# Optimization experiments

Measured on AMD Instinct MI355X. Metric: run time of the kernel, lower is better.

Reference implementation:

```python
import jax, jax.numpy as jnp
import numpy as np

N_ELEC = 8192   # electrons (nodes)
N_NUC = 512     # nuclei
EMB = 256       # embedding_dim
KER = 256       # kernel_dim
DF = 64         # dist_feat_dim
MID = 128       # round(sqrt(DF*KER)), log-interpolated hidden width of w-MLP
E = 131072      # edges per edge type


def _ssp(x):
    # shifted softplus, deepqmc default activation: log(0.5*exp(x) + 0.5)
    return jax.nn.softplus(x) - jnp.log(2.0)


def setup_inputs() -> dict:
    key = jax.random.key(0)
    ks = jax.random.split(key, 24)
    def nrm(k, shape, scale):
        return jax.random.normal(k, shape, dtype=jnp.float32) * scale
    inp = {}
    inp['electrons'] = nrm(ks[0], (N_ELEC, EMB), 1.0)
    inp['nuclei'] = nrm(ks[1], (N_NUC, KER), 1.0)
    for i, lbl in enumerate(['same', 'anti', 'n']):
        inp[f'dist_{lbl}'] = jax.random.uniform(ks[2 + i], (E, DF), dtype=jnp.float32)
        inp[f'w1_{lbl}'] = nrm(ks[5 + i], (DF, MID), DF ** -0.5)
        inp[f'b1_{lbl}'] = jnp.zeros((MID,), jnp.float32)
        inp[f'w2_{lbl}'] = nrm(ks[8 + i], (MID, KER), MID ** -0.5)
        inp[f'g_{lbl}'] = nrm(ks[11 + i], (KER, EMB), KER ** -0.5)
    inp['h_w'] = nrm(ks[14], (EMB, KER), EMB ** -0.5)
    inp['senders_same'] = jax.random.randint(ks[15], (E,), 0, N_ELEC)
    inp['senders_anti'] = jax.random.randint(ks[16], (E,), 0, N_ELEC)
    inp['senders_n'] = jax.random.randint(ks[17], (E,), 0, N_NUC)
    inp['receivers_same'] = jax.random.randint(ks[18], (E,), 0, N_ELEC)
    inp['receivers_anti'] = jax.random.randint(ks[19], (E,), 0, N_ELEC)
    inp['receivers_n'] = jax.random.randint(ks[20], (E,), 0, N_ELEC)
    return inp


def reference(electrons, nuclei, dist_same, dist_anti, dist_n,
              w1_same, b1_same, w2_same, w1_anti, b1_anti, w2_anti,
              w1_n, b1_n, w2_n, g_same, g_anti, g_n, h_w,
              senders_same, senders_anti, senders_n,
              receivers_same, receivers_anti, receivers_n):
    def w_mlp(d, w1, b1, w2):
        # MLP with ('log', 2) hidden layers: linear+bias -> SSP -> last linear (no bias)
        return _ssp(d @ w1 + b1) @ w2

    # per-edge filters from distance features: [E, KER]
    we_same = w_mlp(dist_same, w1_same, b1_same, w2_same)
    we_anti = w_mlp(dist_anti, w1_anti, b1_anti, w2_anti)
    we_n = w_mlp(dist_n, w1_n, b1_n, w2_n)

    # shared h (single bias-free linear) on gathered sender electrons: [E, KER]
    hx_same = electrons[senders_same] @ h_w
    hx_anti = electrons[senders_anti] @ h_w

    weh_same = we_same * hx_same
    weh_anti = we_anti * hx_anti
    weh_n = we_n * nuclei[senders_n]

    # scatter-sum messages to receiver electrons: [N_ELEC, KER]
    z_same = jax.ops.segment_sum(weh_same, receivers_same, num_segments=N_ELEC)
    z_anti = jax.ops.segment_sum(weh_anti, receivers_anti, num_segments=N_ELEC)
    z_n = jax.ops.segment_sum(weh_n, receivers_n, num_segments=N_ELEC)

    # per-label g (single bias-free linear) + residual update, order matches original
    return electrons + (z_n @ g_n + z_same @ g_same + z_anti @ g_anti)
```

## Files before the change

### kernel.cpp

```cpp
#include <hip/hip_runtime.h>
#include <stdint.h>


#define N_ELEC 8192
#define N_NUC  512
#define EMB    256
#define KER    256
#define DF     64
#define MID    128
#define NEDGE  131072
#define RPS    8256
#define CSTR   272

using u16 = unsigned short;
typedef short short8 __attribute__((ext_vector_type(8)));
typedef float f32x4 __attribute__((ext_vector_type(4)));

__device__ __forceinline__ float bf2f(u16 h) {
  return __uint_as_float(((unsigned)h) << 16);
}
__device__ __forceinline__ u16 f2bf(float f) {
  unsigned u = __float_as_uint(f);
  return (u16)((u + 0x7FFFu + ((u >> 16) & 1u)) >> 16);
}
__device__ __forceinline__ unsigned pkbf(float a, float b) {
  return ((unsigned)f2bf(b) << 16) | (unsigned)f2bf(a);
}
__device__ __forceinline__ float ssp_fast(float x) {
  const float e = __expf(-fabsf(x));
  return fmaxf(x, 0.f) + __logf(fmaf(0.5f, e, 0.5f));
}

__device__ __forceinline__ void stage_t64(const char* g0, long stride,
                                          char* lds, int tid) {
  const int l = tid & 63, w = tid >> 6;
  const int r = w * 16 + (l >> 2);
  const int cb = (l & 3) * 16;
  __builtin_amdgcn_global_load_lds(
      (const __attribute__((address_space(1))) unsigned*)(g0 +
                                                          (long)r * stride +
                                                          cb),
      (__attribute__((address_space(3))) unsigned*)(lds + w * 1024), 16, 0, 0);
}
__device__ __forceinline__ void stage_f64(const float* g0, int stride_e,
                                          int kt, char* lds, int tid) {
#pragma unroll
  for (int k = 0; k < 4; ++k) {
    const int idx2 = k * 256 + tid;
    const int row = idx2 >> 4, cp = idx2 & 15;
    const float2 v = *(const float2*)(g0 + (long)row * stride_e + kt + cp * 2);
    *(unsigned*)(lds + row * 64 + cp * 4) = pkbf(v.x, v.y);
  }
}
template <bool A_F32>
__device__ __forceinline__ void gemm64(const char* A0, long as_bytes,
                                       const float* Af, int as_elems,
                                       const char* B0, long bs, int K,
                                       char* As, char* Bs, f32x4 acc[2][2],
                                       int tid) {
  const int l = tid & 63, lane15 = l & 15, quad = l >> 4, wv = tid >> 6;
  const int mw = (wv >> 1) * 32, nw = (wv & 1) * 32;
  for (int kt = 0; kt < K; kt += 32) {
    if (A_F32)
      stage_f64(Af, as_elems, kt, As, tid);
    else
      stage_t64(A0 + (long)kt * 2, as_bytes, As, tid);
    stage_t64(B0 + (long)kt * 2, bs, Bs, tid);
    __syncthreads();
    short8 af[2], bf[2];
#pragma unroll
    for (int i = 0; i < 2; ++i) {
      af[i] = *(const short8*)(As + (mw + i * 16 + lane15) * 64 + quad * 16);
      bf[i] = *(const short8*)(Bs + (nw + i * 16 + lane15) * 64 + quad * 16);
    }
#pragma unroll
    for (int mi = 0; mi < 2; ++mi)
#pragma unroll
      for (int ni = 0; ni < 2; ++ni)
        acc[mi][ni] = __builtin_amdgcn_mfma_f32_16x16x32_bf16(
            af[mi], bf[ni], acc[mi][ni], 0, 0, 0);
    __syncthreads();
  }
}

__global__ __launch_bounds__(256) void k_zero2(float4* z, int* cnt) {
  const int b = blockIdx.x;
  if (b < 6144)
    z[b * 256 + threadIdx.x] = (float4){0.f, 0.f, 0.f, 0.f};
  else
    cnt[(b - 6144) * 256 + threadIdx.x] = 0;
}

__global__ __launch_bounds__(256) void k_hist(const int* r0, const int* r1,
                                              const int* r2, int* cnt) {
  const int t = blockIdx.z;
  const int* rcv = t == 0 ? r0 : (t == 1 ? r1 : r2);
  const int e = blockIdx.x * 256 + threadIdx.x;
  atomicAdd(&cnt[t * N_ELEC + rcv[e]], 1);
}

__global__ __launch_bounds__(256) void k_scan(const int* cnt, int* rowptr,
                                              int* cursor) {
  const int t = blockIdx.x, tid = threadIdx.x;
  __shared__ int part[256];
  const int* c = cnt + t * N_ELEC;
  int s = 0;
#pragma unroll
  for (int i = 0; i < 32; ++i) s += c[tid * 32 + i];
  part[tid] = s;
  __syncthreads();
  for (int off = 1; off < 256; off <<= 1) {
    int v = (tid >= off) ? part[tid - off] : 0;
    __syncthreads();
    part[tid] += v;
    __syncthreads();
  }
  int run = (tid == 0) ? 0 : part[tid - 1];
  int* rp = rowptr + t * RPS;
  int* cu = cursor + t * N_ELEC;
  for (int i = 0; i < 32; ++i) {
    rp[tid * 32 + i] = run;
    cu[tid * 32 + i] = run;
    run += c[tid * 32 + i];
  }
  if (tid == 255) rp[N_ELEC] = run;
}

__global__ __launch_bounds__(256) void k_place(const int* r0, const int* r1,
                                               const int* r2, const int* s0,
                                               const int* s1, const int* s2,
                                               int* cursor, int* perm,
                                               int* snd_s, int* rcv_s) {
  const int t = blockIdx.z;
  const int* rcv = t == 0 ? r0 : (t == 1 ? r1 : r2);
  const int* snd = t == 0 ? s0 : (t == 1 ? s1 : s2);
  const int e = blockIdx.x * 256 + threadIdx.x;
  const int rr = rcv[e];
  const int pos = atomicAdd(&cursor[t * N_ELEC + rr], 1);
  perm[t * NEDGE + pos] = e;
  snd_s[t * NEDGE + pos] = snd[e];
  rcv_s[t * NEDGE + pos] = rr;
}

__global__ __launch_bounds__(256) void k_prep(
    const float* h_w, const float* w1s, const float* w1a, const float* w1n,
    const float* w2s, const float* w2a, const float* w2n, const float* gs,
    const float* ga, const float* gn, u16* hwT, u16* w1T, u16* w2T, u16* gT) {
  int i = blockIdx.x * 256 + threadIdx.x;
  if (i < 65536) {
    int n = i >> 8, k = i & 255;
    hwT[i] = f2bf(h_w[k * 256 + n]);
    return;
  }
  int j = i - 65536;
  if (j < 24576) {
    int t = j >> 13, jj = j & 8191, n = jj >> 6, k = jj & 63;
    const float* w1 = t == 0 ? w1s : (t == 1 ? w1a : w1n);
    w1T[j] = f2bf(w1[k * 128 + n]);
    return;
  }
  j -= 24576;
  if (j < 98304) {
    int t = j >> 15, jj = j & 32767, n = jj >> 7, k = jj & 127;
    const float* w2 = t == 0 ? w2s : (t == 1 ? w2a : w2n);
    w2T[j] = f2bf(w2[k * 256 + n]);
    return;
  }
  j -= 98304;
  if (j < 196608) {
    int n = j / 768, q = j % 768, t = q >> 8, k = q & 255;
    const float* g = t == 0 ? gs : (t == 1 ? ga : gn);
    gT[j] = f2bf(g[k * 256 + n]);
  }
}

__global__ __launch_bounds__(256) void k_he(const float* elec, const u16* hwT,
                                            u16* he) {
  __shared__ char As[4096], Bs[4096];
  f32x4 acc[2][2];
#pragma unroll
  for (int i = 0; i < 2; ++i)
#pragma unroll
    for (int j = 0; j < 2; ++j) acc[i][j] = (f32x4){0.f, 0.f, 0.f, 0.f};
  const int m0 = blockIdx.x * 64, n0 = blockIdx.y * 64;
  gemm64<true>(nullptr, 0, elec + (long)m0 * 256, 256,
               (const char*)hwT + (long)n0 * 512, 512, 256, As, Bs, acc,
               threadIdx.x);
  const int l = threadIdx.x & 63, lane15 = l & 15, quad = l >> 4,
            wv = threadIdx.x >> 6;
  const int mw = (wv >> 1) * 32, nw = (wv & 1) * 32;
#pragma unroll
  for (int mi = 0; mi < 2; ++mi)
#pragma unroll
    for (int r = 0; r < 4; ++r) {
      const int row = m0 + mw + mi * 16 + quad * 4 + r;
#pragma unroll
      for (int ni = 0; ni < 2; ++ni) {
        const int col = n0 + nw + ni * 16 + lane15;
        he[row * 256 + col] = f2bf(acc[mi][ni][r]);
      }
    }
}

__global__ __launch_bounds__(256, 3) void k_edge(
    const float* d0, const float* d1, const float* d2, const float* b0,
    const float* b1p, const float* b2, const u16* w1T, const u16* w2T,
    const u16* he, const float* nucf, const int* perm, const int* snd_s,
    const int* rcv_s, float* z) {
  __shared__ char buf[128 * CSTR];
  __shared__ int snd_l[128], rcv_l[128];

  const int t = blockIdx.z;
  const int m0 = blockIdx.x * 128;
  const int tid = threadIdx.x;
  const float* dist = t == 0 ? d0 : (t == 1 ? d1 : d2);
  const float* bias = t == 0 ? b0 : (t == 1 ? b1p : b2);
  const u16* w1t = w1T + t * 8192;
  const u16* w2t = w2T + t * 32768;
  const bool is_nuc = (t == 2);

  if (tid < 128)
    snd_l[tid] = snd_s[t * NEDGE + m0 + tid];
  else
    rcv_l[tid - 128] = rcv_s[t * NEDGE + m0 + tid - 128];

  int rows[4];
  const int* pm = perm + t * NEDGE + m0;
#pragma unroll
  for (int s = 0; s < 4; ++s) rows[s] = pm[(s * 256 + tid) >> 3];
#pragma unroll
  for (int j = 0; j < 2; ++j)
#pragma unroll
    for (int s = 0; s < 4; ++s) {
      const int idx = s * 256 + tid, row = idx >> 3, ch = idx & 7;
      const float4 v =
          *(const float4*)(dist + (long)rows[s] * 64 + j * 32 + ch * 4);
      uint2 p;
      p.x = pkbf(v.x, v.y);
      p.y = pkbf(v.z, v.w);
      *(uint2*)(buf + j * 8192 + row * 64 + ch * 8) = p;
    }
  __syncthreads();

  const int l = tid & 63, lane15 = l & 15, quad = l >> 4, wv = tid >> 6;
  const int mw = (wv >> 1) * 64, nw = (wv & 1) * 64;

  f32x4 acc[4][4];
#pragma unroll
  for (int i = 0; i < 4; ++i)
#pragma unroll
    for (int j = 0; j < 4; ++j) acc[i][j] = (f32x4){0.f, 0.f, 0.f, 0.f};
#pragma unroll
  for (int j = 0; j < 2; ++j) {
    short8 af[4], bf[4];
#pragma unroll
    for (int i = 0; i < 4; ++i) {
      af[i] = *(const short8*)(buf + j * 8192 + (mw + i * 16 + lane15) * 64 +
                               quad * 16);
      bf[i] = *(const short8*)(w1t + (nw + i * 16 + lane15) * 64 + j * 32 +
                               quad * 8);
    }
#pragma unroll
    for (int mi = 0; mi < 4; ++mi)
#pragma unroll
      for (int ni = 0; ni < 4; ++ni)
        acc[mi][ni] = __builtin_amdgcn_mfma_f32_16x16x32_bf16(
            af[mi], bf[ni], acc[mi][ni], 0, 0, 0);
  }
  __syncthreads();

#pragma unroll
  for (int mi = 0; mi < 4; ++mi)
#pragma unroll
    for (int r = 0; r < 4; ++r) {
      const int row = mw + mi * 16 + quad * 4 + r;
#pragma unroll
      for (int ni = 0; ni < 4; ++ni) {
        const int col = nw + ni * 16 + lane15;
        const float x = acc[mi][ni][r] + bias[col];
        *(u16*)(buf + row * CSTR + col * 2) = f2bf(ssp_fast(x));
      }
    }
  __syncthreads();

  short8 afr[4][4];
#pragma unroll
  for (int j = 0; j < 4; ++j)
#pragma unroll
    for (int i = 0; i < 4; ++i)
      afr[j][i] = *(const short8*)(buf + (mw + i * 16 + lane15) * CSTR +
                                   j * 64 + quad * 16);
  __syncthreads();

  u16* HeC = (u16*)buf;
  for (int n0 = 0; n0 < 256; n0 += 128) {
#pragma unroll
    for (int i = 0; i < 4; ++i)
#pragma unroll
      for (int j = 0; j < 4; ++j) acc[i][j] = (f32x4){0.f, 0.f, 0.f, 0.f};
#pragma unroll
    for (int j = 0; j < 4; ++j) {
      short8 bf[4];
#pragma unroll
      for (int i = 0; i < 4; ++i)
        bf[i] = *(const short8*)(w2t + (n0 + nw + i * 16 + lane15) * 128 +
                                 j * 32 + quad * 8);
#pragma unroll
      for (int mi = 0; mi < 4; ++mi)
#pragma unroll
        for (int ni = 0; ni < 4; ++ni)
          acc[mi][ni] = __builtin_amdgcn_mfma_f32_16x16x32_bf16(
              afr[j][mi], bf[ni], acc[mi][ni], 0, 0, 0);
    }

    if (!is_nuc) {
#pragma unroll
      for (int c = 0; c < 8; ++c) {
        const int chunk = c * 256 + tid;
        const int row = chunk >> 4, off = chunk & 15;
        const uint4 v =
            *(const uint4*)((const char*)he + (size_t)snd_l[row] * 512 +
                            n0 * 2 + off * 16);
        *(uint4*)((char*)HeC + row * CSTR + off * 16) = v;
      }
    } else {
#pragma unroll
      for (int c = 0; c < 8; ++c) {
        const int chunk = c * 256 + tid;
        const int row = chunk >> 4, off = chunk & 15;
        const char* src =
            (const char*)nucf + (size_t)snd_l[row] * 1024 + n0 * 4 + off * 32;
        const float4 a = *(const float4*)src;
        const float4 b = *(const float4*)(src + 16);
        uint4 p;
        p.x = pkbf(a.x, a.y);
        p.y = pkbf(a.z, a.w);
        p.z = pkbf(b.x, b.y);
        p.w = pkbf(b.z, b.w);
        *(uint4*)((char*)HeC + row * CSTR + off * 16) = p;
      }
    }
    __syncthreads();

#pragma unroll
    for (int mi = 0; mi < 4; ++mi)
#pragma unroll
      for (int r = 0; r < 4; ++r) {
        const int row = mw + mi * 16 + quad * 4 + r;
#pragma unroll
        for (int ni = 0; ni < 4; ++ni) {
          const int col = nw + ni * 16 + lane15;
          u16* p = (u16*)((char*)HeC + row * CSTR) + col;
          *p = f2bf(acc[mi][ni][r] * bf2f(*p));
        }
      }
    __syncthreads();

    {
      const int cp = l;
      const int rbeg = wv * 32, rend = rbeg + 32;
      float a0 = 0.f, a1 = 0.f;
      int cur = rcv_l[rbeg];
      for (int row = rbeg; row < rend; ++row) {
        const unsigned p =
            *(const unsigned*)((char*)HeC + row * CSTR + cp * 4);
        a0 += __uint_as_float(p << 16);
        a1 += __uint_as_float(p & 0xffff0000u);
        const int nxt = (row + 1 < rend) ? rcv_l[row + 1] : -1;
        if (nxt != cur) {
          float* zp = z + (size_t)cur * 768 + t * 256 + n0 + cp * 2;
          unsafeAtomicAdd(zp, a0);
          unsafeAtomicAdd(zp + 1, a1);
          a0 = a1 = 0.f;
          cur = nxt;
        }
      }
    }
    __syncthreads();
  }
}

__global__ __launch_bounds__(256) void k_final(const float* z, const u16* gT,
                                               const float* elec, float* out) {
  __shared__ char As[4096], Bs[4096];
  f32x4 acc[2][2];
#pragma unroll
  for (int i = 0; i < 2; ++i)
#pragma unroll
    for (int j = 0; j < 2; ++j) acc[i][j] = (f32x4){0.f, 0.f, 0.f, 0.f};
  const int m0 = blockIdx.x * 64, n0 = blockIdx.y * 64;
  gemm64<true>(nullptr, 0, z + (long)m0 * 768, 768,
               (const char*)gT + (long)n0 * 1536, 1536, 768, As, Bs, acc,
               threadIdx.x);
  const int l = threadIdx.x & 63, lane15 = l & 15, quad = l >> 4,
            wv = threadIdx.x >> 6;
  const int mw = (wv >> 1) * 32, nw = (wv & 1) * 32;
#pragma unroll
  for (int mi = 0; mi < 2; ++mi)
#pragma unroll
    for (int r = 0; r < 4; ++r) {
      const int row = m0 + mw + mi * 16 + quad * 4 + r;
#pragma unroll
      for (int ni = 0; ni < 2; ++ni) {
        const int col = n0 + nw + ni * 16 + lane15;
        out[row * 256 + col] = acc[mi][ni][r] + elec[row * 256 + col];
      }
    }
}

extern "C" void kernel_launch(void* const* d_in, const int* in_sizes, int n_in,
                              void* d_out, int out_size, void* d_ws,
                              size_t ws_size, hipStream_t stream) {
  int I_dist[3], I_w1[3], I_b1[3], I_w2[3], I_g[3], I_hw;
  if (in_sizes[3] == 64 * 128) {
    for (int t = 0; t < 3; ++t) {
      I_dist[t] = 2 + t * 5 + 0;
      I_w1[t] = 2 + t * 5 + 1;
      I_b1[t] = 2 + t * 5 + 2;
      I_w2[t] = 2 + t * 5 + 3;
      I_g[t] = 2 + t * 5 + 4;
    }
    I_hw = 17;
  } else {
    I_dist[0] = 2; I_dist[1] = 3; I_dist[2] = 4;
    I_w1[0] = 5;  I_b1[0] = 6;  I_w2[0] = 7;
    I_w1[1] = 8;  I_b1[1] = 9;  I_w2[1] = 10;
    I_w1[2] = 11; I_b1[2] = 12; I_w2[2] = 13;
    I_g[0] = 14; I_g[1] = 15; I_g[2] = 16;
    I_hw = 17;
  }
  const int I_snd[3] = {18, 19, 20};
  const int I_rcv[3] = {21, 22, 23};

  char* ws = (char*)d_ws;
  u16* he = (u16*)(ws + 0);
  u16* hwT = (u16*)(ws + 4194304);
  u16* w1T = (u16*)(ws + 4325376);
  u16* w2T = (u16*)(ws + 4374528);
  u16* gT = (u16*)(ws + 4571136);
  float* z = (float*)(ws + 4964352);
  int* cnt = (int*)(ws + 30130176);
  int* rowptr = (int*)(ws + 30228480);
  int* cursor = (int*)(ws + 30327552);
  int* perm = (int*)(ws + 30425856);
  int* snd_s = (int*)(ws + 31998720);
  int* rcv_s = (int*)(ws + 33571584);

  const float* elec = (const float*)d_in[0];
  const float* nuc = (const float*)d_in[1];
  const int* s0 = (const int*)d_in[I_snd[0]];
  const int* s1 = (const int*)d_in[I_snd[1]];
  const int* s2 = (const int*)d_in[I_snd[2]];
  const int* r0 = (const int*)d_in[I_rcv[0]];
  const int* r1 = (const int*)d_in[I_rcv[1]];
  const int* r2 = (const int*)d_in[I_rcv[2]];

  k_zero2<<<6240, 256, 0, stream>>>((float4*)z, cnt);

  k_hist<<<dim3(NEDGE / 256, 1, 3), 256, 0, stream>>>(r0, r1, r2, cnt);
  k_scan<<<3, 256, 0, stream>>>(cnt, rowptr, cursor);
  k_place<<<dim3(NEDGE / 256, 1, 3), 256, 0, stream>>>(r0, r1, r2, s0, s1, s2,
                                                       cursor, perm, snd_s,
                                                       rcv_s);

  k_prep<<<1504, 256, 0, stream>>>(
      (const float*)d_in[I_hw], (const float*)d_in[I_w1[0]],
      (const float*)d_in[I_w1[1]], (const float*)d_in[I_w1[2]],
      (const float*)d_in[I_w2[0]], (const float*)d_in[I_w2[1]],
      (const float*)d_in[I_w2[2]], (const float*)d_in[I_g[0]],
      (const float*)d_in[I_g[1]], (const float*)d_in[I_g[2]], hwT, w1T, w2T,
      gT);

  k_he<<<dim3(N_ELEC / 64, 4), 256, 0, stream>>>(elec, hwT, he);

  k_edge<<<dim3(NEDGE / 128, 1, 3), 256, 0, stream>>>(
      (const float*)d_in[I_dist[0]], (const float*)d_in[I_dist[1]],
      (const float*)d_in[I_dist[2]], (const float*)d_in[I_b1[0]],
      (const float*)d_in[I_b1[1]], (const float*)d_in[I_b1[2]], w1T, w2T, he,
      nuc, perm, snd_s, rcv_s, z);

  k_final<<<dim3(N_ELEC / 64, 4), 256, 0, stream>>>(z, gT, elec,
                                                    (float*)d_out);
}
```

Measured before the change: 457.0 us.

## Fuse weight prep into zero kernel and restructure edge kernel second GEMM staging

Merges the weight transpose/convert kernel into the zeroing kernel, removing one launch. In the edge kernel, the SSP hidden activations stay in their own LDS buffer and A fragments are reloaded per k-step instead of being held in 64 registers. The gathered sender features are staged in a separate 64-row buffer in two halves, with only the owning waves multiplying. This lowers register pressure, possibly raising occupancy, but adds LDS traffic, more barriers and halves gather parallelism per step.

```diff
diff --git a/kernel.cpp b/kernel.cpp
--- a/kernel.cpp
+++ b/kernel.cpp
@@ -83,12 +83,46 @@
   }
 }
 
-__global__ __launch_bounds__(256) void k_zero2(float4* z, int* cnt) {
+__global__ __launch_bounds__(256) void k_setup(
+    const float* h_w, const float* w1s, const float* w1a, const float* w1n,
+    const float* w2s, const float* w2a, const float* w2n, const float* gs,
+    const float* ga, const float* gn, u16* hwT, u16* w1T, u16* w2T, u16* gT,
+    float4* z, int* cnt) {
   const int b = blockIdx.x;
-  if (b < 6144)
+  if (b < 6144) {
     z[b * 256 + threadIdx.x] = (float4){0.f, 0.f, 0.f, 0.f};
-  else
+    return;
+  }
+  if (b < 6240) {
     cnt[(b - 6144) * 256 + threadIdx.x] = 0;
+    return;
+  }
+  int i = (b - 6240) * 256 + threadIdx.x;
+  if (i < 65536) {
+    int n = i >> 8, k = i & 255;
+    hwT[i] = f2bf(h_w[k * 256 + n]);
+    return;
+  }
+  int j = i - 65536;
+  if (j < 24576) {
+    int t = j >> 13, jj = j & 8191, n = jj >> 6, k = jj & 63;
+    const float* w1 = t == 0 ? w1s : (t == 1 ? w1a : w1n);
+    w1T[j] = f2bf(w1[k * 128 + n]);
+    return;
+  }
+  j -= 24576;
+  if (j < 98304) {
+    int t = j >> 15, jj = j & 32767, n = jj >> 7, k = jj & 127;
+    const float* w2 = t == 0 ? w2s : (t == 1 ? w2a : w2n);
+    w2T[j] = f2bf(w2[k * 256 + n]);
+    return;
+  }
+  j -= 98304;
+  if (j < 196608) {
+    int n = j / 768, q = j % 768, t = q >> 8, k = q & 255;
+    const float* g = t == 0 ? gs : (t == 1 ? ga : gn);
+    gT[j] = f2bf(g[k * 256 + n]);
+  }
 }
 
 __global__ __launch_bounds__(256) void k_hist(const int* r0, const int* r1,
@@ -142,38 +176,6 @@
   rcv_s[t * NEDGE + pos] = rr;
 }
 
-__global__ __launch_bounds__(256) void k_prep(
-    const float* h_w, const float* w1s, const float* w1a, const float* w1n,
-    const float* w2s, const float* w2a, const float* w2n, const float* gs,
-    const float* ga, const float* gn, u16* hwT, u16* w1T, u16* w2T, u16* gT) {
-  int i = blockIdx.x * 256 + threadIdx.x;
-  if (i < 65536) {
-    int n = i >> 8, k = i & 255;
-    hwT[i] = f2bf(h_w[k * 256 + n]);
-    return;
-  }
-  int j = i - 65536;
-  if (j < 24576) {
-    int t = j >> 13, jj = j & 8191, n = jj >> 6, k = jj & 63;
-    const float* w1 = t == 0 ? w1s : (t == 1 ? w1a : w1n);
-    w1T[j] = f2bf(w1[k * 128 + n]);
-    return;
-  }
-  j -= 24576;
-  if (j < 98304) {
-    int t = j >> 15, jj = j & 32767, n = jj >> 7, k = jj & 127;
-    const float* w2 = t == 0 ? w2s : (t == 1 ? w2a : w2n);
-    w2T[j] = f2bf(w2[k * 256 + n]);
-    return;
-  }
-  j -= 98304;
-  if (j < 196608) {
-    int n = j / 768, q = j % 768, t = q >> 8, k = q & 255;
-    const float* g = t == 0 ? gs : (t == 1 ? ga : gn);
-    gT[j] = f2bf(g[k * 256 + n]);
-  }
-}
-
 __global__ __launch_bounds__(256) void k_he(const float* elec, const u16* hwT,
                                             u16* he) {
   __shared__ char As[4096], Bs[4096];
@@ -207,7 +209,8 @@
     const float* b1p, const float* b2, const u16* w1T, const u16* w2T,
     const u16* he, const float* nucf, const int* perm, const int* snd_s,
     const int* rcv_s, float* z) {
-  __shared__ char buf[128 * CSTR];
+  __shared__ char mid[128 * CSTR];
+  __shared__ char hc[64 * CSTR];
   __shared__ int snd_l[128], rcv_l[128];
 
   const int t = blockIdx.z;
@@ -238,7 +241,7 @@
       uint2 p;
       p.x = pkbf(v.x, v.y);
       p.y = pkbf(v.z, v.w);
-      *(uint2*)(buf + j * 8192 + row * 64 + ch * 8) = p;
+      *(uint2*)(mid + j * 8192 + row * 64 + ch * 8) = p;
     }
   __syncthreads();
 
@@ -255,7 +258,7 @@
     short8 af[4], bf[4];
 #pragma unroll
     for (int i = 0; i < 4; ++i) {
-      af[i] = *(const short8*)(buf + j * 8192 + (mw + i * 16 + lane15) * 64 +
+      af[i] = *(const short8*)(mid + j * 8192 + (mw + i * 16 + lane15) * 64 +
                                quad * 16);
       bf[i] = *(const short8*)(w1t + (nw + i * 16 + lane15) * 64 + j * 32 +
                                quad * 8);
@@ -278,105 +281,104 @@
       for (int ni = 0; ni < 4; ++ni) {
         const int col = nw + ni * 16 + lane15;
         const float x = acc[mi][ni][r] + bias[col];
-        *(u16*)(buf + row * CSTR + col * 2) = f2bf(ssp_fast(x));
+        *(u16*)(mid + row * CSTR + col * 2) = f2bf(ssp_fast(x));
       }
     }
   __syncthreads();
 
-  short8 afr[4][4];
-#pragma unroll
-  for (int j = 0; j < 4; ++j)
+  for (int n0 = 0; n0 < 256; n0 += 128) {
 #pragma unroll
     for (int i = 0; i < 4; ++i)
-      afr[j][i] = *(const short8*)(buf + (mw + i * 16 + lane15) * CSTR +
-                                   j * 64 + quad * 16);
-  __syncthreads();
-
-  u16* HeC = (u16*)buf;
-  for (int n0 = 0; n0 < 256; n0 += 128) {
-#pragma unroll
-    for (int i = 0; i < 4; ++i)
 #pragma unroll
       for (int j = 0; j < 4; ++j) acc[i][j] = (f32x4){0.f, 0.f, 0.f, 0.f};
 #pragma unroll
-    for (int j = 0; j < 4; ++j) {
-      short8 bf[4];
-#pragma unroll
-      for (int i = 0; i < 4; ++i)
-        bf[i] = *(const short8*)(w2t + (n0 + nw + i * 16 + lane15) * 128 +
-                                 j * 32 + quad * 8);
+    for (int kt = 0; kt < 128; kt += 32) {
+      short8 af[4], bf[4];
+#pragma unroll
+      for (int i = 0; i < 4; ++i) {
+        af[i] = *(const short8*)(mid + (mw + i * 16 + lane15) * CSTR + kt * 2 +
+                                 quad * 16);
+        bf[i] = *(const short8*)(w2t + (n0 + nw + i * 16 + lane15) * 128 + kt +
+                                 quad * 8);
+      }
 #pragma unroll
       for (int mi = 0; mi < 4; ++mi)
 #pragma unroll
         for (int ni = 0; ni < 4; ++ni)
           acc[mi][ni] = __builtin_amdgcn_mfma_f32_16x16x32_bf16(
-              afr[j][mi], bf[ni], acc[mi][ni], 0, 0, 0);
-    }
-
-    if (!is_nuc) {
-#pragma unroll
-      for (int c = 0; c < 8; ++c) {
-        const int chunk = c * 256 + tid;
-        const int row = chunk >> 4, off = chunk & 15;
-        const uint4 v =
-            *(const uint4*)((const char*)he + (size_t)snd_l[row] * 512 +
-                            n0 * 2 + off * 16);
-        *(uint4*)((char*)HeC + row * CSTR + off * 16) = v;
-      }
-    } else {
-#pragma unroll
-      for (int c = 0; c < 8; ++c) {
-        const int chunk = c * 256 + tid;
-        const int row = chunk >> 4, off = chunk & 15;
-        const char* src =
-            (const char*)nucf + (size_t)snd_l[row] * 1024 + n0 * 4 + off * 32;
-        const float4 a = *(const float4*)src;
-        const float4 b = *(const float4*)(src + 16);
-        uint4 p;
-        p.x = pkbf(a.x, a.y);
-        p.y = pkbf(a.z, a.w);
-        p.z = pkbf(b.x, b.y);
-        p.w = pkbf(b.z, b.w);
-        *(uint4*)((char*)HeC + row * CSTR + off * 16) = p;
-      }
-    }
-    __syncthreads();
-
-#pragma unroll
-    for (int mi = 0; mi < 4; ++mi)
-#pragma unroll
-      for (int r = 0; r < 4; ++r) {
-        const int row = mw + mi * 16 + quad * 4 + r;
-#pragma unroll
-        for (int ni = 0; ni < 4; ++ni) {
-          const int col = nw + ni * 16 + lane15;
-          u16* p = (u16*)((char*)HeC + row * CSTR) + col;
-          *p = f2bf(acc[mi][ni][r] * bf2f(*p));
+              af[mi], bf[ni], acc[mi][ni], 0, 0, 0);
+    }
+
+    for (int h = 0; h < 2; ++h) {
+      const int rbase = h * 64;
+      if (!is_nuc) {
+#pragma unroll
+        for (int c = 0; c < 4; ++c) {
+          const int chunk = c * 256 + tid;
+          const int row = chunk >> 4, off = chunk & 15;
+          const uint4 v =
+              *(const uint4*)((const char*)he +
+                              (size_t)snd_l[rbase + row] * 512 + n0 * 2 +
+                              off * 16);
+          *(uint4*)(hc + row * CSTR + off * 16) = v;
         }
-      }
-    __syncthreads();
-
-    {
-      const int cp = l;
-      const int rbeg = wv * 32, rend = rbeg + 32;
-      float a0 = 0.f, a1 = 0.f;
-      int cur = rcv_l[rbeg];
-      for (int row = rbeg; row < rend; ++row) {
-        const unsigned p =
-            *(const unsigned*)((char*)HeC + row * CSTR + cp * 4);
-        a0 += __uint_as_float(p << 16);
-        a1 += __uint_as_float(p & 0xffff0000u);
-        const int nxt = (row + 1 < rend) ? rcv_l[row + 1] : -1;
-        if (nxt != cur) {
-          float* zp = z + (size_t)cur * 768 + t * 256 + n0 + cp * 2;
-          unsafeAtomicAdd(zp, a0);
-          unsafeAtomicAdd(zp + 1, a1);
-          a0 = a1 = 0.f;
-          cur = nxt;
+      } else {
+#pragma unroll
+        for (int c = 0; c < 4; ++c) {
+          const int chunk = c * 256 + tid;
+          const int row = chunk >> 4, off = chunk & 15;
+          const char* src = (const char*)nucf +
+                            (size_t)snd_l[rbase + row] * 1024 + n0 * 4 +
+                            off * 32;
+          const float4 a = *(const float4*)src;
+          const float4 b = *(const float4*)(src + 16);
+          uint4 p;
+          p.x = pkbf(a.x, a.y);
+          p.y = pkbf(a.z, a.w);
+          p.z = pkbf(b.x, b.y);
+          p.w = pkbf(b.z, b.w);
+          *(uint4*)(hc + row * CSTR + off * 16) = p;
         }
       }
-    }
-    __syncthreads();
+      __syncthreads();
+
+      if ((wv >> 1) == h) {
+#pragma unroll
+        for (int mi = 0; mi < 4; ++mi)
+#pragma unroll
+          for (int r = 0; r < 4; ++r) {
+            const int lrow = mi * 16 + quad * 4 + r;
+#pragma unroll
+            for (int ni = 0; ni < 4; ++ni) {
+              const int col = nw + ni * 16 + lane15;
+              u16* p = (u16*)(hc + lrow * CSTR) + col;
+              *p = f2bf(acc[mi][ni][r] * bf2f(*p));
+            }
+          }
+      }
+      __syncthreads();
+
+      {
+        const int cp = l;
+        const int rbeg = wv * 16, rend = rbeg + 16;
+        float a0 = 0.f, a1 = 0.f;
+        int cur = rcv_l[rbase + rbeg];
+        for (int row = rbeg; row < rend; ++row) {
+          const unsigned p = *(const unsigned*)(hc + row * CSTR + cp * 4);
+          a0 += __uint_as_float(p << 16);
+          a1 += __uint_as_float(p & 0xffff0000u);
+          const int nxt = (row + 1 < rend) ? rcv_l[rbase + row + 1] : -1;
+          if (nxt != cur) {
+            float* zp = z + (size_t)cur * 768 + t * 256 + n0 + cp * 2;
+            unsafeAtomicAdd(zp, a0);
+            unsafeAtomicAdd(zp + 1, a1);
+            a0 = a1 = 0.f;
+            cur = nxt;
+          }
+        }
+      }
+      __syncthreads();
+    }
   }
 }
 
@@ -455,7 +457,13 @@
   const int* r1 = (const int*)d_in[I_rcv[1]];
   const int* r2 = (const int*)d_in[I_rcv[2]];
 
-  k_zero2<<<6240, 256, 0, stream>>>((float4*)z, cnt);
+  k_setup<<<7744, 256, 0, stream>>>(
+      (const float*)d_in[I_hw], (const float*)d_in[I_w1[0]],
+      (const float*)d_in[I_w1[1]], (const float*)d_in[I_w1[2]],
+      (const float*)d_in[I_w2[0]], (const float*)d_in[I_w2[1]],
+      (const float*)d_in[I_w2[2]], (const float*)d_in[I_g[0]],
+      (const float*)d_in[I_g[1]], (const float*)d_in[I_g[2]], hwT, w1T, w2T,
+      gT, (float4*)z, cnt);
 
   k_hist<<<dim3(NEDGE / 256, 1, 3), 256, 0, stream>>>(r0, r1, r2, cnt);
   k_scan<<<3, 256, 0, stream>>>(cnt, rowptr, cursor);
@@ -463,14 +471,6 @@
                                                        cursor, perm, snd_s,
                                                        rcv_s);
 
-  k_prep<<<1504, 256, 0, stream>>>(
-      (const float*)d_in[I_hw], (const float*)d_in[I_w1[0]],
-      (const float*)d_in[I_w1[1]], (const float*)d_in[I_w1[2]],
-      (const float*)d_in[I_w2[0]], (const float*)d_in[I_w2[1]],
-      (const float*)d_in[I_w2[2]], (const float*)d_in[I_g[0]],
-      (const float*)d_in[I_g[1]], (const float*)d_in[I_g[2]], hwT, w1T, w2T,
-      gT);
-
   k_he<<<dim3(N_ELEC / 64, 4), 256, 0, stream>>>(elec, hwT, he);
 
   k_edge<<<dim3(NEDGE / 128, 1, 3), 256, 0, stream>>>(
```

Measured after the change: 404.9 us. -11.4%, faster.
